# Kernel tuning notes

Hardware: AMD Instinct MI355X
Metric: run time of the kernel (lower is better)

The kernel has to match this reference:

```python
import jax, jax.numpy as jnp
import numpy as np

NUM_FRAMES = 8
NUM_CLASSES = 40
INNER_TH = 0.5
MIN_WH = 0.05
SUPPRESS = 1e9


def _xyxy_to_cxcywh(b):
    x1, y1, x2, y2 = b[..., 0], b[..., 1], b[..., 2], b[..., 3]
    return jnp.stack([(x1 + x2) * 0.5, (y1 + y2) * 0.5, x2 - x1, y2 - y1], -1)


def setup_inputs() -> dict:
    key = jax.random.key(0)
    k1, k2, k3, k4, k5 = jax.random.split(key, 5)
    B, N, T = 4, 20, NUM_FRAMES
    H = W = 160
    # valid xyxy boxes: centers in [0.1,0.9], wh in [0.02,0.3]
    c = jax.random.uniform(k1, (B, N, T, 2), minval=0.1, maxval=0.9)
    wh = jax.random.uniform(k2, (B, N, T, 2), minval=0.02, maxval=0.3)
    gt_boxes = jnp.concatenate([c - wh / 2, c + wh / 2], -1).astype(jnp.float32)
    gt_labels = jax.random.randint(k3, (B, N), 0, NUM_CLASSES)
    ids = jax.random.randint(k4, (B, N, T), 0, 100)
    drop = jax.random.bernoulli(k5, 0.1, (B, N, T))
    gt_ids = jnp.where(drop, -1, ids)  # -1 => instance absent in that frame
    ys, xs = jnp.meshgrid(jnp.arange(H), jnp.arange(W), indexing='ij')
    ref_points = jnp.stack([(xs.reshape(-1) + 0.5) / W, (ys.reshape(-1) + 0.5) / H], -1).astype(jnp.float32)
    spatial_shapes = jnp.array([H, W], dtype=jnp.int32)
    return dict(gt_labels=gt_labels, gt_boxes=gt_boxes, gt_ids=gt_ids,
                ref_points=ref_points, spatial_shapes=spatial_shapes)


def _match_frame(dist_t, ids_t, labels, valid):
    # dist_t [N,P], ids_t [N], labels [N], valid [N]; sequential suppression over n
    N, P = dist_t.shape
    arangeP = jnp.arange(P)
    arangeC = jnp.arange(NUM_CLASSES)

    def step(carry, n):
        d_all, ml, md, mi = carry
        d = d_all[n]                                   # [P]
        act = valid[n] & (ids_t[n] != -1)
        inner = d < INNER_TH
        # if no inner point, claim just the single closest point
        pos = jnp.where(inner.any(), inner, arangeP == jnp.argmin(d)) & act
        lab = labels[n]
        score = 1.0 - 2.0 * jnp.clip(d, 0.0, INNER_TH)
        ml = jnp.where(pos, lab, ml)
        md = jnp.where(pos[:, None] & (arangeC == lab)[None, :], score[:, None], md)
        mi = jnp.where(pos, ids_t[n], mi)
        d_all = jnp.where(pos[None, :], SUPPRESS, d_all)  # suppress claimed points for all gts
        return (d_all, ml, md, mi), None

    init = (dist_t,
            jnp.full((P,), -1, jnp.int32),
            jnp.zeros((P, NUM_CLASSES), dist_t.dtype),
            jnp.full((P,), -1, jnp.int32))
    (_, ml, md, mi), _ = jax.lax.scan(step, init, jnp.arange(N))
    return ml, md, mi


def reference(gt_labels, gt_boxes, gt_ids, ref_points, spatial_shapes):
    B, N, T, _ = gt_boxes.shape
    boxes_c = _xyxy_to_cxcywh(gt_boxes)                 # [B,N,T,4]
    area = (boxes_c[..., 2] * boxes_c[..., 3]).mean(-1)  # [B,N] mean area over frames
    order = jnp.argsort(area, axis=1)                   # process small instances first
    boxes_c = jnp.take_along_axis(boxes_c, order[:, :, None, None], axis=1)
    labels = jnp.take_along_axis(gt_labels.astype(jnp.int32), order, axis=1)
    ids = jnp.take_along_axis(gt_ids.astype(jnp.int32), order[:, :, None], axis=1)
    valid = (boxes_c[..., 2:] > 0.0).all(-1).any(-1) & (labels >= 0)  # [B,N]
    # normalized center distance: [B,N,T,P]
    diff = (boxes_c[..., None, :2] - ref_points[None, None, None, :, :]) / jnp.clip(boxes_c[..., None, 2:], MIN_WH)
    dist = jnp.sum(diff ** 2, -1)
    f = jax.vmap(jax.vmap(_match_frame, in_axes=(1, 1, None, None)), in_axes=(0, 0, 0, 0))
    ml, md, mi = f(dist, ids, labels, valid)            # [B,T,P], [B,T,P,C], [B,T,P]
    return ml, md, mi
```

## Files before the change

### kernel.cpp

```cpp
#include <hip/hip_runtime.h>

#define BB   4
#define NGT  20
#define TT   8
#define PP   25600
#define CC   40
#define TPB  1024
#define SUPP 1e9f
#define INNER_TH 0.5f
#define FILLB 224

#define PK_CLAIM  1u
#define PK_LAB_SH 1
#define PK_ID_SH  7
#define PK_MDV    (1u << 14)
#define PK_MDC_SH 15
#define PK_MDN_SH 21

__device__ inline unsigned long long shfl_down_u64(unsigned long long v, int off) {
    unsigned lo = (unsigned)v, hi = (unsigned)(v >> 32);
    lo = __shfl_down(lo, off, 64);
    hi = __shfl_down(hi, off, 64);
    return ((unsigned long long)hi << 32) | (unsigned long long)lo;
}

__device__ inline float4 make_geo(const float* __restrict__ gt_boxes, int b, int n, int t) {
    const float* bx = gt_boxes + ((size_t)(b * NGT + n) * TT + t) * 4;
    float x1 = bx[0], y1 = bx[1], x2 = bx[2], y2 = bx[3];
    float4 g;
    g.x = __fmul_rn(__fadd_rn(x1, x2), 0.5f);
    g.y = __fmul_rn(__fadd_rn(y1, y2), 0.5f);
    g.z = fmaxf(__fsub_rn(x2, x1), 0.05f);
    g.w = fmaxf(__fsub_rn(y2, y1), 0.05f);
    return g;
}

__device__ inline float point_dist(int px, int py, float4 g) {
    float rxv = __fdiv_rn((float)px + 0.5f, 160.0f);
    float ryv = __fdiv_rn((float)py + 0.5f, 160.0f);
    float dx = __fdiv_rn(__fsub_rn(g.x, rxv), g.z);
    float dy = __fdiv_rn(__fsub_rn(g.y, ryv), g.w);
    return __fadd_rn(__fmul_rn(dx, dx), __fmul_rn(dy, dy));
}

__global__ __launch_bounds__(TPB) void match_fill_kernel(
        const int*   __restrict__ gt_labels,
        const float* __restrict__ gt_boxes,
        const int*   __restrict__ gt_ids,
        unsigned* __restrict__ packs_g,
        uint4*    __restrict__ md4) {
    if (blockIdx.x >= BB * TT) {
        const int MD4 = BB * TT * PP * CC / 4;
        const int stride = FILLB * TPB;
        uint4 z = make_uint4(0u, 0u, 0u, 0u);
        for (int i = (blockIdx.x - BB * TT) * TPB + (int)threadIdx.x; i < MD4; i += stride)
            md4[i] = z;
        return;
    }

    int bt = blockIdx.x;
    int b  = bt >> 3;
    int t  = bt & 7;
    int tid = threadIdx.x;

    __shared__ unsigned s_pack[PP];
    __shared__ float  s_dxx[NGT * 160];
    __shared__ float  s_dyy[NGT * 160];
    __shared__ float  s_area[NGT];
    __shared__ int    s_valid[NGT];
    __shared__ int    s_order[NGT];
    __shared__ int    s_any[NGT];
    __shared__ float4 s_geo[NGT];
    __shared__ int4   s_meta[NGT];
    __shared__ int    s_actlist[NGT];
    __shared__ int    s_actcnt;
    __shared__ unsigned long long s_wave[TPB / 64];
    __shared__ unsigned long long s_bcast;

    {
        uint4 z = make_uint4(0u, 0u, 0u, 0u);
        for (int i = tid; i < PP / 4; i += TPB) ((uint4*)s_pack)[i] = z;
    }
    if (tid < NGT) {
        const float* bx = gt_boxes + (size_t)(b * NGT + tid) * TT * 4;
        float a[TT];
        int anyPos = 0;
        for (int f = 0; f < TT; f++) {
            float w = __fsub_rn(bx[f * 4 + 2], bx[f * 4 + 0]);
            float h = __fsub_rn(bx[f * 4 + 3], bx[f * 4 + 1]);
            a[f] = __fmul_rn(w, h);
            anyPos |= (w > 0.0f && h > 0.0f) ? 1 : 0;
        }
        float s = __fadd_rn(__fadd_rn(__fadd_rn(a[0], a[1]), __fadd_rn(a[2], a[3])),
                            __fadd_rn(__fadd_rn(a[4], a[5]), __fadd_rn(a[6], a[7])));
        s_area[tid]  = __fmul_rn(s, 0.125f);
        s_valid[tid] = (anyPos && gt_labels[b * NGT + tid] >= 0) ? 1 : 0;
        s_any[tid]   = 0;
    }
    __syncthreads();

    if (tid < NGT) {
        float an = s_area[tid];
        int r = 0;
        for (int m2 = 0; m2 < NGT; m2++) {
            float am = s_area[m2];
            r += (am < an || (am == an && m2 < tid)) ? 1 : 0;
        }
        s_order[r] = tid;
    }
    __syncthreads();

    if (tid < NGT) {
        int n   = s_order[tid];
        int src = b * NGT + n;
        s_geo[tid] = make_geo(gt_boxes, b, n, t);
        int id = gt_ids[src * TT + t];
        int4 mm;
        mm.x = gt_labels[src];
        mm.y = id;
        mm.z = (s_valid[n] && id != -1) ? 1 : 0;
        mm.w = n;
        s_meta[tid] = mm;
    }
    __syncthreads();
    if (tid == 0) {
        int c = 0;
        for (int k = 0; k < NGT; k++)
            if (s_meta[k].z) s_actlist[c++] = k;
        s_actcnt = c;
    }

    for (int i = tid; i < NGT * 320; i += TPB) {
        int slot = i / 320;
        int w    = i - slot * 320;
        float4 g = s_geo[slot];
        if (w < 160) {
            float rxv = __fdiv_rn((float)w + 0.5f, 160.0f);
            float dx  = __fdiv_rn(__fsub_rn(g.x, rxv), g.z);
            s_dxx[slot * 160 + w] = __fmul_rn(dx, dx);
        } else {
            int py = w - 160;
            float ryv = __fdiv_rn((float)py + 0.5f, 160.0f);
            float dy  = __fdiv_rn(__fsub_rn(g.y, ryv), g.w);
            s_dyy[slot * 160 + py] = __fmul_rn(dy, dy);
        }
    }
    __syncthreads();
    int actcnt = s_actcnt;

    for (int j = 0; j < actcnt; j++) {
        int slot = s_actlist[j];
        int4 m  = s_meta[slot];
        float4 g = s_geo[slot];
        const float* dxx = s_dxx + slot * 160;
        const float* dyy = s_dyy + slot * 160;

        float ex = __fmul_rn(g.z, 0.70711f);
        float ey = __fmul_rn(g.w, 0.70711f);
        int x0 = max(0,   (int)floorf((g.x - ex) * 160.0f - 0.5f) - 1);
        int x1 = min(159, (int)ceilf ((g.x + ex) * 160.0f - 0.5f) + 1);
        int y0 = max(0,   (int)floorf((g.y - ey) * 160.0f - 0.5f) - 1);
        int y1 = min(159, (int)ceilf ((g.y + ey) * 160.0f - 0.5f) + 1);
        int rw = x1 - x0 + 1;
        int M  = rw * (y1 - y0 + 1);

        unsigned base = PK_CLAIM | ((unsigned)m.x << PK_LAB_SH) |
                        ((unsigned)m.y << PK_ID_SH) | PK_MDV |
                        ((unsigned)m.x << PK_MDC_SH) |
                        ((unsigned)m.w << PK_MDN_SH);
        int found = 0;
        {
            int r  = tid / rw;
            int c  = tid - r * rw;
            int dr = TPB / rw;
            int dc = TPB - dr * rw;
            for (int i = tid; i < M; i += TPB) {
                int px = x0 + c;
                int py = y0 + r;
                int p  = py * 160 + px;
                if (!(s_pack[p] & PK_CLAIM)) {
                    float d = __fadd_rn(dxx[px], dyy[py]);
                    if (d < INNER_TH) {
                        s_pack[p] = base;
                        found = 1;
                    }
                }
                c += dc; r += dr;
                if (c >= rw) { c -= rw; r++; }
            }
        }
        if (found) s_any[j] = 1;
        __syncthreads();

        if (!s_any[j]) {
            unsigned long long key = ~0ULL;
            {
                int py = tid / 160;
                int px = tid - py * 160;
                for (int p = tid; p < PP; p += TPB) {
                    float deff;
                    if (s_pack[p] & PK_CLAIM) {
                        deff = SUPP;
                    } else {
                        deff = __fadd_rn(dxx[px], dyy[py]);
                    }
                    unsigned long long kk =
                        ((unsigned long long)__float_as_uint(deff) << 32) |
                        (unsigned long long)(unsigned)p;
                    key = (kk < key) ? kk : key;
                    px += 64; py += 6;
                    if (px >= 160) { px -= 160; py++; }
                }
            }
            unsigned long long v = key;
            for (int off = 32; off > 0; off >>= 1) {
                unsigned long long o = shfl_down_u64(v, off);
                v = (o < v) ? o : v;
            }
            int lane = tid & 63, wave = tid >> 6;
            if (lane == 0) s_wave[wave] = v;
            __syncthreads();
            if (tid == 0) {
                unsigned long long mval = s_wave[0];
                for (int w = 1; w < TPB / 64; w++) mval = (s_wave[w] < mval) ? s_wave[w] : mval;
                s_bcast = mval;
            }
            __syncthreads();
            unsigned long long gmin = s_bcast;
            float minv = __uint_as_float((unsigned)(gmin >> 32));
            int minp = (int)(unsigned)(gmin & 0xffffffffu);
            if ((minp & (TPB - 1)) == tid) {
                unsigned npk = PK_CLAIM | ((unsigned)m.x << PK_LAB_SH) |
                               ((unsigned)m.y << PK_ID_SH);
                if (minv < SUPP) {
                    s_pack[minp] = npk;
                } else {
                    unsigned old = s_pack[minp];
                    unsigned mdbits = old & (PK_MDV | (63u << PK_MDC_SH) | (31u << PK_MDN_SH));
                    if ((old & PK_MDV) &&
                        ((old >> PK_MDC_SH) & 63u) == (unsigned)m.x) mdbits = 0u;
                    s_pack[minp] = npk | mdbits;
                }
            }
            __syncthreads();
        }
    }

    __syncthreads();
    uint4* dst = (uint4*)(packs_g + (size_t)bt * PP);
    for (int i = tid; i < PP / 4; i += TPB) dst[i] = ((const uint4*)s_pack)[i];
}

__global__ __launch_bounds__(256) void scatter_kernel(
        const unsigned* __restrict__ packs,
        const float*    __restrict__ gt_boxes,
        float* __restrict__ out) {
    const int    ML = BB * TT * PP;
    const size_t MD = (size_t)BB * TT * PP * CC;
    int f = blockIdx.x * 256 + threadIdx.x;
    uint4 pk4 = ((const uint4*)packs)[f];

    float4 vml, vmi;
    vml.x = (pk4.x & PK_CLAIM) ? (float)((pk4.x >> PK_LAB_SH) & 63u) : -1.0f;
    vml.y = (pk4.y & PK_CLAIM) ? (float)((pk4.y >> PK_LAB_SH) & 63u) : -1.0f;
    vml.z = (pk4.z & PK_CLAIM) ? (float)((pk4.z >> PK_LAB_SH) & 63u) : -1.0f;
    vml.w = (pk4.w & PK_CLAIM) ? (float)((pk4.w >> PK_LAB_SH) & 63u) : -1.0f;
    vmi.x = (pk4.x & PK_CLAIM) ? (float)((pk4.x >> PK_ID_SH) & 127u) : -1.0f;
    vmi.y = (pk4.y & PK_CLAIM) ? (float)((pk4.y >> PK_ID_SH) & 127u) : -1.0f;
    vmi.z = (pk4.z & PK_CLAIM) ? (float)((pk4.z >> PK_ID_SH) & 127u) : -1.0f;
    vmi.w = (pk4.w & PK_CLAIM) ? (float)((pk4.w >> PK_ID_SH) & 127u) : -1.0f;
    ((float4*)out)[f] = vml;
    ((float4*)(out + ML + MD))[f] = vmi;

    int pt0 = f << 2;
#pragma unroll
    for (int k = 0; k < 4; k++) {
        unsigned pk = (k == 0) ? pk4.x : (k == 1) ? pk4.y : (k == 2) ? pk4.z : pk4.w;
        if (pk & PK_MDV) {
            int pt  = pt0 + k;
            int cls = (int)((pk >> PK_MDC_SH) & 63u);
            int n   = (int)((pk >> PK_MDN_SH) & 31u);
            int bt  = pt / PP;
            int p   = pt - bt * PP;
            int py  = p / 160;
            int px  = p - py * 160;
            float4 g = make_geo(gt_boxes, bt >> 3, n, bt & 7);
            float d  = point_dist(px, py, g);
            out[ML + (size_t)pt * CC + cls] = __fsub_rn(1.0f, __fmul_rn(2.0f, d));
        }
    }
}

extern "C" void kernel_launch(void* const* d_in, const int* in_sizes, int n_in,
                              void* d_out, int out_size, void* d_ws, size_t ws_size,
                              hipStream_t stream) {
    const int*   gt_labels = (const int*)d_in[0];
    const float* gt_boxes  = (const float*)d_in[1];
    const int*   gt_ids    = (const int*)d_in[2];

    unsigned* packs = (unsigned*)d_ws;
    float*    outf  = (float*)d_out;

    match_fill_kernel<<<BB * TT + FILLB, TPB, 0, stream>>>(
        gt_labels, gt_boxes, gt_ids, packs,
        (uint4*)(outf + BB * TT * PP));

    scatter_kernel<<<(BB * TT * PP / 4) / 256, 256, 0, stream>>>(packs, gt_boxes, outf);
}
```

Before: 168.8 us.

## Use per-row claimed bitmask to find argmin fallback without full scan

Adds a shared bitmask of claimed points, updated whenever a point is claimed. The fallback argmin for instances with no inner points now has each of 160 threads search one row, using bit scans to find the nearest unclaimed columns around the box centre instead of scanning all 25600 points. This removes a full-image pass per fallback instance, at the cost of atomics in the inner-claim loop and more complex tie-breaking logic.

```diff
diff --git a/kernel.cpp b/kernel.cpp
--- a/kernel.cpp
+++ b/kernel.cpp
@@ -64,6 +64,7 @@
     int tid = threadIdx.x;
 
     __shared__ unsigned s_pack[PP];
+    __shared__ unsigned s_mask[160 * 5];
     __shared__ float  s_dxx[NGT * 160];
     __shared__ float  s_dyy[NGT * 160];
     __shared__ float  s_area[NGT];
@@ -81,6 +82,7 @@
         uint4 z = make_uint4(0u, 0u, 0u, 0u);
         for (int i = tid; i < PP / 4; i += TPB) ((uint4*)s_pack)[i] = z;
     }
+    if (tid < 160 * 5) s_mask[tid] = 0u;
     if (tid < NGT) {
         const float* bx = gt_boxes + (size_t)(b * NGT + tid) * TT * 4;
         float a[TT];
@@ -182,6 +184,7 @@
                     float d = __fadd_rn(dxx[px], dyy[py]);
                     if (d < INNER_TH) {
                         s_pack[p] = base;
+                        atomicOr(&s_mask[p >> 5], 1u << (p & 31));
                         found = 1;
                     }
                 }
@@ -194,22 +197,82 @@
 
         if (!s_any[j]) {
             unsigned long long key = ~0ULL;
-            {
-                int py = tid / 160;
-                int px = tid - py * 160;
-                for (int p = tid; p < PP; p += TPB) {
-                    float deff;
-                    if (s_pack[p] & PK_CLAIM) {
-                        deff = SUPP;
-                    } else {
-                        deff = __fadd_rn(dxx[px], dyy[py]);
-                    }
-                    unsigned long long kk =
-                        ((unsigned long long)__float_as_uint(deff) << 32) |
-                        (unsigned long long)(unsigned)p;
-                    key = (kk < key) ? kk : key;
-                    px += 64; py += 6;
-                    if (px >= 160) { px -= 160; py++; }
+            if (tid < 160) {
+                int y = tid;
+                unsigned um[5];
+#pragma unroll
+                for (int w = 0; w < 5; w++) um[w] = ~s_mask[y * 5 + w];
+                unsigned anyu = um[0] | um[1] | um[2] | um[3] | um[4];
+                if (!anyu) {
+                    if (y == 0)
+                        key = ((unsigned long long)__float_as_uint(SUPP) << 32);
+                } else {
+                    float dyyv = dyy[y];
+                    int xs = (int)floorf(__fsub_rn(__fmul_rn(g.x, 160.0f), 0.5f));
+                    xs = min(max(xs, -2), 161);
+                    float bd = 2e9f;
+                    int   bx = -1;
+#pragma unroll
+                    for (int k2 = 0; k2 < 2; k2++) {
+                        int x = xs + k2;
+                        if (x >= 0 && x <= 159 && ((um[x >> 5] >> (x & 31)) & 1u)) {
+                            float d2 = __fadd_rn(dxx[x], dyyv);
+                            if (d2 < bd || (d2 == bd && x < bx)) { bd = d2; bx = x; }
+                        }
+                    }
+                    {
+                        int xq = min(xs - 1, 159);
+                        int xL = -1;
+                        if (xq >= 0) {
+                            int w = xq >> 5;
+                            unsigned mm = um[w] & (0xffffffffu >> (31 - (xq & 31)));
+                            while (true) {
+                                if (mm) { xL = (w << 5) + (31 - __clz(mm)); break; }
+                                if (--w < 0) break;
+                                mm = um[w];
+                            }
+                        }
+                        if (xL >= 0) {
+                            float dL = __fadd_rn(dxx[xL], dyyv);
+                            while (xL > 0) {
+                                int xq2 = xL - 1;
+                                int w = xq2 >> 5;
+                                unsigned mm = um[w] & (0xffffffffu >> (31 - (xq2 & 31)));
+                                int x2 = -1;
+                                while (true) {
+                                    if (mm) { x2 = (w << 5) + (31 - __clz(mm)); break; }
+                                    if (--w < 0) break;
+                                    mm = um[w];
+                                }
+                                if (x2 < 0) break;
+                                if (__fadd_rn(dxx[x2], dyyv) != dL) break;
+                                xL = x2;
+                            }
+                            if (dL < bd || (dL == bd && xL < bx)) { bd = dL; bx = xL; }
+                        }
+                    }
+                    {
+                        int xq = max(xs + 2, 0);
+                        int xR = -1;
+                        if (xq <= 159) {
+                            int w = xq >> 5;
+                            unsigned mm = um[w] & (0xffffffffu << (xq & 31));
+                            while (true) {
+                                if (mm) { xR = (w << 5) + (__ffs(mm) - 1); break; }
+                                if (++w > 4) break;
+                                mm = um[w];
+                            }
+                        }
+                        if (xR >= 0) {
+                            float dR = __fadd_rn(dxx[xR], dyyv);
+                            if (dR < bd || (dR == bd && xR < bx)) { bd = dR; bx = xR; }
+                        }
+                    }
+                    if (bx >= 0) {
+                        int p = y * 160 + bx;
+                        key = ((unsigned long long)__float_as_uint(bd) << 32) |
+                              (unsigned long long)(unsigned)p;
+                    }
                 }
             }
             unsigned long long v = key;
@@ -241,6 +304,7 @@
                         ((old >> PK_MDC_SH) & 63u) == (unsigned)m.x) mdbits = 0u;
                     s_pack[minp] = npk | mdbits;
                 }
+                atomicOr(&s_mask[minp >> 5], 1u << (minp & 31));
             }
             __syncthreads();
         }
```

Measured after the change: 165.3 us. 2.1% less time.
